# Kernel optimization log

Measured on AMD Instinct MI355X. Metric: run time of the kernel, lower is better.

The kernel has to match this reference:

```python
import jax, jax.numpy as jnp
import numpy as np

THRESHOLDS = jnp.array([0.5, 1.0, 1.5, 2.0, 3.0], dtype=jnp.float32)

B, E, D = 4096, 64, 256


def setup_inputs() -> dict:
    key = jax.random.key(0)
    k1, k2, k3 = jax.random.split(key, 3)
    predicted = jax.random.normal(k1, (B, D), dtype=jnp.float32)
    entity_vectors = jax.random.normal(k2, (B, E, D), dtype=jnp.float32)
    entity_mask = jax.random.randint(k3, (B, E, 2), 0, 2, dtype=jnp.int32)
    return {"predicted": predicted, "entity_vectors": entity_vectors, "entity_mask": entity_mask}


def _acc_counts(predicted, entity_vectors, entity_mask):
    # mask column 0, as in torch: entity_mask[:, 0].bool()
    mask = entity_mask[:, :, 0].astype(bool)                      # [B, E]
    is_known = mask[:, 0]                                         # [B]
    # negatives = masked-selected vectors with the FIRST selected one dropped
    # (torch: entity_vectors[mask][1:]) -> exclude first True position
    cum = jnp.cumsum(mask.astype(jnp.int32), axis=1)
    neg_mask = mask & (cum > 1)                                   # [B, E]
    has_neg = jnp.any(neg_mask, axis=1)                           # [B]

    # Euclidean distances
    pos_dist = jnp.linalg.norm(entity_vectors[:, 0, :] - predicted, axis=-1)      # [B]
    all_dist = jnp.linalg.norm(entity_vectors - predicted[:, None, :], axis=-1)   # [B, E]
    min_neg = jnp.min(jnp.where(neg_mask, all_dist, jnp.inf), axis=1)             # [B]

    # category index: (is_known, has_negatives) -> 0..3
    idx = is_known.astype(jnp.int32) * 2 + has_neg.astype(jnp.int32)              # [B]
    onehot = jax.nn.one_hot(idx, 4, dtype=jnp.float32)                            # [B, 4]
    entity_counts = jnp.sum(onehot, axis=0).reshape(2, 2)                         # [known, has_neg]

    t = THRESHOLDS[:, None]                                                        # [T, 1]
    known = is_known[None, :]
    hn = has_neg[None, :]
    pos = pos_dist[None, :]
    mn = min_neg[None, :]
    # incorrect-prediction flags per threshold, per the original branch logic
    flags = jnp.where(
        known & ~hn, t < pos,
        jnp.where(~known & hn, mn < t,
                  jnp.where(known & hn, jnp.minimum(mn, t) < pos, False)))        # [T, B]
    incorrect = (flags.astype(jnp.float32) @ onehot).reshape(-1, 2, 2)            # [T, 2, 2]
    return entity_counts, incorrect


def reference(predicted, entity_vectors, entity_mask):
    entity_counts, incorrect = _acc_counts(predicted, entity_vectors, entity_mask)
    return entity_counts.astype(jnp.int32), incorrect.astype(jnp.int32)
```

## Files before the change

kernel.cpp:

```cpp
#include <hip/hip_runtime.h>
#include <math.h>

#define NB 4096
#define NE 64
#define ND 256
#define ROWS_PER_BLOCK 4
#define NBLOCKS (NB / ROWS_PER_BLOCK)

__global__ __launch_bounds__(256) void acc_kernel(
    const float* __restrict__ pred,
    const float* __restrict__ ev,
    const int* __restrict__ em,
    int* __restrict__ out)
{
    __shared__ float dist2[NE];
    __shared__ int lcnt[24];
    const int tid  = threadIdx.x;
    const int wave = tid >> 6;
    const int lane = tid & 63;

    if (tid < 24) lcnt[tid] = 0;
    __syncthreads();

    for (int j = 0; j < ROWS_PER_BLOCK; ++j) {
        const int b = blockIdx.x * ROWS_PER_BLOCK + j;

        const float4 p = ((const float4*)pred)[(size_t)b * (ND / 4) + lane];
        const float4* evb = (const float4*)ev + (size_t)b * NE * (ND / 4);

        #pragma unroll
        for (int i = 0; i < 16; ++i) {
            const int e = wave * 16 + i;
            const float4 v = evb[e * (ND / 4) + lane];
            const float dx = v.x - p.x, dy = v.y - p.y;
            const float dz = v.z - p.z, dw = v.w - p.w;
            float s = dx * dx + dy * dy + dz * dz + dw * dw;
            #pragma unroll
            for (int off = 32; off > 0; off >>= 1)
                s += __shfl_xor(s, off, 64);
            if (lane == 0) dist2[e] = s;
        }
        __syncthreads();

        if (wave == 0) {
            const bool m = em[((size_t)b * NE + lane) * 2] != 0;
            const unsigned long long bm = __ballot(m);
            const bool known = (bm & 1ull) != 0ull;
            const bool hn    = (bm & (bm - 1ull)) != 0ull;
            const int  first = __ffsll(bm) - 1;
            const bool neg   = m && (lane != first);

            float mn2 = neg ? dist2[lane] : INFINITY;
            #pragma unroll
            for (int off = 32; off > 0; off >>= 1)
                mn2 = fminf(mn2, __shfl_xor(mn2, off, 64));

            if (lane == 0) {
                const float pos2 = dist2[0];
                const int idx = (known ? 2 : 0) + (hn ? 1 : 0);
                lcnt[idx] += 1;
                const float t2[5] = {0.25f, 1.0f, 2.25f, 4.0f, 9.0f};
                #pragma unroll
                for (int t = 0; t < 5; ++t) {
                    bool flag = false;
                    if (known && !hn)      flag = t2[t] < pos2;
                    else if (!known && hn) flag = mn2 < t2[t];
                    else if (known && hn)  flag = fminf(mn2, t2[t]) < pos2;
                    if (flag) lcnt[4 + t * 4 + idx] += 1;
                }
            }
        }
        __syncthreads();
    }

    if (tid < 24 && lcnt[tid] != 0) atomicAdd(&out[tid], lcnt[tid]);
}

extern "C" void kernel_launch(void* const* d_in, const int* in_sizes, int n_in,
                              void* d_out, int out_size, void* d_ws, size_t ws_size,
                              hipStream_t stream) {
    const float* pred = (const float*)d_in[0];
    const float* ev   = (const float*)d_in[1];
    const int*   em   = (const int*)d_in[2];
    int* out = (int*)d_out;

    hipMemsetAsync(out, 0, out_size * sizeof(int), stream);
    acc_kernel<<<NBLOCKS, 256, 0, stream>>>(pred, ev, em, out);
}
```

Measured before the change: 363.2 us.

## Load only masked negative and positive entity vectors, dropping per-row syncs

Reads the mask first and computes distances only for entity rows that count as negatives, spread round-robin across the four waves, plus row 0 only when the row is known. Unmasked entity vectors are never loaded from memory. Per-row barriers are replaced by per-wave partial minima in shared memory, with a single reduction step after all rows. Rows per block drop from 4 to 2. This cuts memory traffic roughly in half for random masks, at the cost of data-dependent loops that cause wave imbalance and scattered row reads.

Result: faster. 345.9 us (-4.8%).

```diff
diff --git a/kernel.cpp b/kernel.cpp
--- a/kernel.cpp
+++ b/kernel.cpp
@@ -3,9 +3,9 @@
 
 #define NB 4096
 #define NE 64
-#define ND 256
-#define ROWS_PER_BLOCK 4
-#define NBLOCKS (NB / ROWS_PER_BLOCK)
+#define ND4 64
+#define RPB 2
+#define NBLOCKS (NB / RPB)
 
 __global__ __launch_bounds__(256) void acc_kernel(
     const float* __restrict__ pred,
@@ -13,65 +13,82 @@
     const int* __restrict__ em,
     int* __restrict__ out)
 {
-    __shared__ float dist2[NE];
-    __shared__ int lcnt[24];
+    __shared__ float wmin[RPB][4];
+    __shared__ float wpos[RPB];
+    __shared__ int   kn[RPB], hn[RPB];
+    __shared__ int   lcnt[24];
+
     const int tid  = threadIdx.x;
     const int wave = tid >> 6;
     const int lane = tid & 63;
 
     if (tid < 24) lcnt[tid] = 0;
-    __syncthreads();
 
-    for (int j = 0; j < ROWS_PER_BLOCK; ++j) {
-        const int b = blockIdx.x * ROWS_PER_BLOCK + j;
+    for (int j = 0; j < RPB; ++j) {
+        const int b = blockIdx.x * RPB + j;
+        const float4  p   = ((const float4*)pred)[(size_t)b * ND4 + lane];
+        const float4* evb = (const float4*)ev + (size_t)b * NE * ND4;
 
-        const float4 p = ((const float4*)pred)[(size_t)b * (ND / 4) + lane];
-        const float4* evb = (const float4*)ev + (size_t)b * NE * (ND / 4);
+        const bool m = em[((size_t)b * NE + lane) * 2] != 0;
+        const unsigned long long bm = __ballot(m);
+        const bool known = (bm & 1ull) != 0ull;
+        const unsigned long long nm = bm & (bm - 1ull);
 
-        #pragma unroll
-        for (int i = 0; i < 16; ++i) {
-            const int e = wave * 16 + i;
-            const float4 v = evb[e * (ND / 4) + lane];
+        unsigned long long mynm = nm;
+        for (int i = 0; i < wave && mynm; ++i) mynm &= mynm - 1ull;
+
+        float mn2 = INFINITY;
+        while (mynm) {
+            const int e = (int)__ffsll(mynm) - 1;
+            const float4 v = evb[(size_t)e * ND4 + lane];
             const float dx = v.x - p.x, dy = v.y - p.y;
             const float dz = v.z - p.z, dw = v.w - p.w;
-            float s = dx * dx + dy * dy + dz * dz + dw * dw;
+            float s = dx*dx + dy*dy + dz*dz + dw*dw;
             #pragma unroll
             for (int off = 32; off > 0; off >>= 1)
                 s += __shfl_xor(s, off, 64);
-            if (lane == 0) dist2[e] = s;
+            mn2 = fminf(mn2, s);
+            #pragma unroll
+            for (int i = 0; i < 4; ++i) mynm &= mynm - 1ull;
         }
-        __syncthreads();
+        if (lane == 0) wmin[j][wave] = mn2;
 
         if (wave == 0) {
-            const bool m = em[((size_t)b * NE + lane) * 2] != 0;
-            const unsigned long long bm = __ballot(m);
-            const bool known = (bm & 1ull) != 0ull;
-            const bool hn    = (bm & (bm - 1ull)) != 0ull;
-            const int  first = __ffsll(bm) - 1;
-            const bool neg   = m && (lane != first);
+            if (known) {
+                const float4 v = evb[lane];
+                const float dx = v.x - p.x, dy = v.y - p.y;
+                const float dz = v.z - p.z, dw = v.w - p.w;
+                float s = dx*dx + dy*dy + dz*dz + dw*dw;
+                #pragma unroll
+                for (int off = 32; off > 0; off >>= 1)
+                    s += __shfl_xor(s, off, 64);
+                if (lane == 0) wpos[j] = s;
+            }
+            if (lane == 0) { kn[j] = known; hn[j] = (nm != 0ull); }
+        }
+    }
+    __syncthreads();
 
-            float mn2 = neg ? dist2[lane] : INFINITY;
-            #pragma unroll
-            for (int off = 32; off > 0; off >>= 1)
-                mn2 = fminf(mn2, __shfl_xor(mn2, off, 64));
-
-            if (lane == 0) {
-                const float pos2 = dist2[0];
-                const int idx = (known ? 2 : 0) + (hn ? 1 : 0);
-                lcnt[idx] += 1;
-                const float t2[5] = {0.25f, 1.0f, 2.25f, 4.0f, 9.0f};
-                #pragma unroll
-                for (int t = 0; t < 5; ++t) {
-                    bool flag = false;
-                    if (known && !hn)      flag = t2[t] < pos2;
-                    else if (!known && hn) flag = mn2 < t2[t];
-                    else if (known && hn)  flag = fminf(mn2, t2[t]) < pos2;
-                    if (flag) lcnt[4 + t * 4 + idx] += 1;
-                }
-            }
+    if (tid < RPB) {
+        const int j = tid;
+        const bool known = kn[j] != 0;
+        const bool hneg  = hn[j] != 0;
+        const float mn2  = fminf(fminf(wmin[j][0], wmin[j][1]),
+                                 fminf(wmin[j][2], wmin[j][3]));
+        const float pos2 = known ? wpos[j] : 0.f;
+        const int idx = (known ? 2 : 0) + (hneg ? 1 : 0);
+        atomicAdd(&lcnt[idx], 1);
+        const float t2[5] = {0.25f, 1.0f, 2.25f, 4.0f, 9.0f};
+        #pragma unroll
+        for (int t = 0; t < 5; ++t) {
+            bool flag = false;
+            if (known && !hneg)      flag = t2[t] < pos2;
+            else if (!known && hneg) flag = mn2 < t2[t];
+            else if (known && hneg)  flag = fminf(mn2, t2[t]) < pos2;
+            if (flag) atomicAdd(&lcnt[4 + t * 4 + idx], 1);
         }
-        __syncthreads();
     }
+    __syncthreads();
 
     if (tid < 24 && lcnt[tid] != 0) atomicAdd(&out[tid], lcnt[tid]);
 }
```
